# Performance work log

Measured on AMD Instinct MI355X. Metric: run time of the kernel, lower is better.

Reference implementation:

```python
import jax, jax.numpy as jnp
import numpy as np

N, IN, D, H, L, G, FF, E = 50000, 100, 128, 8, 3, 64, 512, 800000


def setup_inputs() -> dict:
    key = jax.random.key(0)
    ks = jax.random.split(key, 12)
    s = 0.02
    x = jax.random.normal(ks[0], (N, IN), dtype=jnp.float32)
    edge_index = jax.random.randint(ks[1], (2, E), 0, N)
    batch = jnp.sort(jax.random.randint(ks[2], (N,), 0, G))
    emb_W = jax.random.normal(ks[3], (IN, D), dtype=jnp.float32) * s
    Wqk = jax.random.normal(ks[4], (L, D, 2 * D), dtype=jnp.float32) * s
    Wv = jax.random.normal(ks[5], (L, D, D), dtype=jnp.float32) * s
    Wo = jax.random.normal(ks[6], (L, D, D), dtype=jnp.float32) * s
    bo = jnp.zeros((L, D), dtype=jnp.float32)
    W1 = jax.random.normal(ks[7], (L, D, FF), dtype=jnp.float32) * s
    b1 = jnp.zeros((L, FF), dtype=jnp.float32)
    W2 = jax.random.normal(ks[8], (L, FF, D), dtype=jnp.float32) * s
    b2 = jnp.zeros((L, D), dtype=jnp.float32)
    return {"x": x, "emb_W": emb_W, "Wqk": Wqk, "Wv": Wv, "Wo": Wo, "bo": bo,
            "W1": W1, "b1": b1, "W2": W2, "b2": b2,
            "edge_index": edge_index, "batch": batch}


def reference(x, emb_W, Wqk, Wv, Wo, bo, W1, b1, W2, b2, edge_index, batch):
    n = x.shape[0]
    d = emb_W.shape[1]
    n_layers = Wqk.shape[0]
    n_heads = H
    hd = d // n_heads
    scale = hd ** (-0.5)
    src, dst = edge_index[0], edge_index[1]  # PyG: j=source, i=target

    h = x @ emb_W  # [n, d]  (dropout is identity in eval)
    for l in range(n_layers):
        qk = h @ Wqk[l]  # [n, 2d]; chunk0 -> _j (source), chunk1 -> _i (target)
        q = qk[:, :d].reshape(n, n_heads, hd)
        k = qk[:, d:].reshape(n, n_heads, hd)
        v = (h @ Wv[l]).reshape(n, n_heads, hd)
        # per-edge attention scores [E, H]
        scores = jnp.sum(k[dst] * q[src], axis=-1) * scale
        # segment softmax over edges sharing a destination node
        m = jax.ops.segment_max(scores, dst, num_segments=n)
        ex = jnp.exp(scores - m[dst])
        denom = jax.ops.segment_sum(ex, dst, num_segments=n)
        attn = ex / (denom[dst] + 1e-16)  # utils.softmax adds 1e-16
        msg = v[src] * attn[:, :, None]  # [E, H, hd]
        out = jax.ops.segment_sum(msg, dst, num_segments=n).reshape(n, d)
        out = out @ Wo[l] + bo[l]
        h = h + out  # norm1 = Identity (batch_norm=True)
        ff = jax.nn.relu(h @ W1[l] + b1[l]) @ W2[l] + b2[l]
        h = h + ff  # norm2 = Identity
    # global mean pool per graph
    n_graphs = G
    sums = jax.ops.segment_sum(h, batch, num_segments=n_graphs)
    cnt = jax.ops.segment_sum(jnp.ones((n, 1), h.dtype), batch, num_segments=n_graphs)
    return sums / jnp.maximum(cnt, 1.0)
```

## Files before the change

kernel.cpp:

```cpp
#include <hip/hip_runtime.h>
#include <math.h>

#define NN 50000
#define NPAD 50048
#define IN_DIM 100
#define DD 128
#define HH 8
#define LL 3
#define GG 64
#define FFD 512
#define EE 800000

typedef __attribute__((ext_vector_type(8))) short bf8_t;
typedef __attribute__((ext_vector_type(4))) float f4_t;

static __device__ __forceinline__ unsigned short f2bf(float f) {
    unsigned u = __builtin_bit_cast(unsigned, f);
    unsigned r = (u + 0x7FFFu + ((u >> 16) & 1u)) >> 16;
    return (unsigned short)r;
}
static __device__ __forceinline__ float bf2f(unsigned short b) {
    unsigned u = ((unsigned)b) << 16;
    return __builtin_bit_cast(float, u);
}

#define GLD16(gsrc, ldst) __builtin_amdgcn_global_load_lds( \
    (const __attribute__((address_space(1))) unsigned int*)(gsrc), \
    (__attribute__((address_space(3))) unsigned int*)(ldst), 16, 0, 0)

__global__ __launch_bounds__(256) void mfma_gemm(
    const unsigned short* __restrict__ Ac,
    const unsigned short* __restrict__ Bc,
    const float* __restrict__ bias,
    const float* __restrict__ resid,
    float* __restrict__ Cf,
    unsigned short* __restrict__ Chl,
    unsigned short* __restrict__ Cb,
    int n, int nk, int M, int do_relu, int a_plain)
{
    __shared__ unsigned short ldsA[128 * 64];
    __shared__ unsigned short ldsB[128 * 64];
    const int tid = threadIdx.x;
    const int lane = tid & 63;
    const int wid = tid >> 6;
    const int wr = (wid >> 1) * 64;
    const int wc = (wid & 1) * 64;
    const long brow = (long)blockIdx.x * 128;
    const long bcol = (long)blockIdx.y * 128;

    f4_t acc[4][4] = {};

    const int srow = tid >> 3;
    const int kbg = (((tid & 7) << 4) ^ ((srow & 7) << 4)) >> 1;
    const int fr = lane & 15;
    const int kq = (lane >> 4) << 4;
    const int kq4 = lane >> 4;

    for (int kc = 0; kc < nk; ++kc) {
        if (a_plain) {
#pragma unroll
            for (int i = 0; i < 2; ++i) {
                int lin = i * 256 + tid;
                int row = lin >> 2, sd = lin & 3;
                GLD16(Ac + (brow + row) * (size_t)(nk * 32) + kc * 32 + ((sd ^ (row & 3)) << 3),
                      &ldsA[(size_t)lin * 8]);
            }
        } else {
#pragma unroll
            for (int i = 0; i < 4; ++i) {
                int row = i * 32 + srow;
                GLD16(Ac + ((brow + row) * (size_t)nk + kc) * 64 + kbg,
                      &ldsA[((size_t)i * 256 + tid) * 8]);
            }
        }
#pragma unroll
        for (int i = 0; i < 4; ++i) {
            int row = i * 32 + srow;
            GLD16(Bc + ((bcol + row) * (size_t)nk + kc) * 64 + kbg,
                  &ldsB[((size_t)i * 256 + tid) * 8]);
        }
        __syncthreads();

        bf8_t bh[4], bl[4];
#pragma unroll
        for (int nn = 0; nn < 4; ++nn) {
            int row = wc + nn * 16 + fr;
            int sw = (row & 7) << 4;
            bh[nn] = *(const bf8_t*)&ldsB[row * 64 + ((kq ^ sw) >> 1)];
            bl[nn] = *(const bf8_t*)&ldsB[row * 64 + (((kq + 64) ^ sw) >> 1)];
        }
        if (a_plain) {
            bf8_t ah[4];
#pragma unroll
            for (int m = 0; m < 4; ++m) {
                int row = wr + m * 16 + fr;
                ah[m] = *(const bf8_t*)&ldsA[row * 32 + ((kq4 ^ (row & 3)) << 3)];
            }
#pragma unroll
            for (int m = 0; m < 4; ++m)
#pragma unroll
                for (int nn = 0; nn < 4; ++nn) {
                    acc[m][nn] = __builtin_amdgcn_mfma_f32_16x16x32_bf16(ah[m], bh[nn], acc[m][nn], 0, 0, 0);
                    acc[m][nn] = __builtin_amdgcn_mfma_f32_16x16x32_bf16(ah[m], bl[nn], acc[m][nn], 0, 0, 0);
                }
        } else {
            bf8_t ah[4], al[4];
#pragma unroll
            for (int m = 0; m < 4; ++m) {
                int row = wr + m * 16 + fr;
                int sw = (row & 7) << 4;
                ah[m] = *(const bf8_t*)&ldsA[row * 64 + ((kq ^ sw) >> 1)];
                al[m] = *(const bf8_t*)&ldsA[row * 64 + (((kq + 64) ^ sw) >> 1)];
            }
#pragma unroll
            for (int m = 0; m < 4; ++m)
#pragma unroll
                for (int nn = 0; nn < 4; ++nn) {
                    acc[m][nn] = __builtin_amdgcn_mfma_f32_16x16x32_bf16(ah[m], bh[nn], acc[m][nn], 0, 0, 0);
                    acc[m][nn] = __builtin_amdgcn_mfma_f32_16x16x32_bf16(al[m], bh[nn], acc[m][nn], 0, 0, 0);
                    acc[m][nn] = __builtin_amdgcn_mfma_f32_16x16x32_bf16(ah[m], bl[nn], acc[m][nn], 0, 0, 0);
                }
        }
        __syncthreads();
    }

    const int efr = lane & 15, efq = lane >> 4;
#pragma unroll
    for (int m = 0; m < 4; ++m) {
#pragma unroll
        for (int i = 0; i < 4; ++i) {
            long row = brow + wr + m * 16 + efq * 4 + i;
            if (row >= n) continue;
#pragma unroll
            for (int nn = 0; nn < 4; ++nn) {
                int col = (int)bcol + wc + nn * 16 + efr;
                float v = acc[m][nn][i];
                if (bias) v += bias[col];
                if (do_relu) v = fmaxf(v, 0.f);
                if (resid) v += resid[row * M + col];
                if (Cf) Cf[row * M + col] = v;
                if (Cb) Cb[row * M + col] = f2bf(v);
                if (Chl) {
                    unsigned short hb = f2bf(v);
                    float lo = v - bf2f(hb);
                    size_t cb = (row * (size_t)(M >> 5) + (col >> 5)) * 64 + (col & 31);
                    Chl[cb] = hb;
                    Chl[cb + 32] = f2bf(lo);
                }
            }
        }
    }
}

__global__ __launch_bounds__(256, 3) void ff_fused(
    const unsigned short* __restrict__ hcin,
    const unsigned short* __restrict__ W1T,
    const unsigned short* __restrict__ W2T,
    const float* __restrict__ b1,
    const float* __restrict__ b2,
    float* __restrict__ h,
    unsigned short* __restrict__ hcout,
    int n)
{
    __shared__ unsigned short ldsA[64 * 32];
    __shared__ unsigned short ldsB[128 * 64];
    __shared__ unsigned short midb[64 * 128];

    const int tid = threadIdx.x;
    const int lane = tid & 63;
    const int wid = tid >> 6;
    const int wr = (wid >> 1) * 32;
    const int wc = (wid & 1) * 64;
    const long brow = (long)blockIdx.x * 64;

    const int srow = tid >> 3;
    const int kbg = (((tid & 7) << 4) ^ ((srow & 7) << 4)) >> 1;
    const int fr = lane & 15;
    const int kq = (lane >> 4) << 4;
    const int kq4 = lane >> 4;
    const int efr = lane & 15, efq = lane >> 4;

    f4_t acc2[2][4] = {};

    for (int c = 0; c < 4; ++c) {
        f4_t acc1[2][4] = {};
        for (int kc = 0; kc < 4; ++kc) {
            {
                int row = tid >> 2, sd = tid & 3;
                GLD16(hcin + ((brow + row) * (size_t)4 + kc) * 64 + ((sd ^ (row & 3)) << 3),
                      &ldsA[(size_t)tid * 8]);
            }
#pragma unroll
            for (int i = 0; i < 4; ++i) {
                int row = i * 32 + srow;
                GLD16(W1T + (((size_t)c * 128 + row) * 4 + kc) * 64 + kbg,
                      &ldsB[((size_t)i * 256 + tid) * 8]);
            }
            __syncthreads();
            bf8_t ah[2], bh[4], bl[4];
#pragma unroll
            for (int m = 0; m < 2; ++m) {
                int row = wr + m * 16 + fr;
                ah[m] = *(const bf8_t*)&ldsA[row * 32 + ((kq4 ^ (row & 3)) << 3)];
            }
#pragma unroll
            for (int nn = 0; nn < 4; ++nn) {
                int rowb = wc + nn * 16 + fr;
                int sw = (rowb & 7) << 4;
                bh[nn] = *(const bf8_t*)&ldsB[rowb * 64 + ((kq ^ sw) >> 1)];
                bl[nn] = *(const bf8_t*)&ldsB[rowb * 64 + (((kq + 64) ^ sw) >> 1)];
            }
#pragma unroll
            for (int m = 0; m < 2; ++m)
#pragma unroll
                for (int nn = 0; nn < 4; ++nn) {
                    acc1[m][nn] = __builtin_amdgcn_mfma_f32_16x16x32_bf16(ah[m], bh[nn], acc1[m][nn], 0, 0, 0);
                    acc1[m][nn] = __builtin_amdgcn_mfma_f32_16x16x32_bf16(ah[m], bl[nn], acc1[m][nn], 0, 0, 0);
                }
            __syncthreads();
        }
#pragma unroll
        for (int m = 0; m < 2; ++m)
#pragma unroll
            for (int i = 0; i < 4; ++i) {
                int lrow = wr + m * 16 + efq * 4 + i;
#pragma unroll
                for (int nn = 0; nn < 4; ++nn) {
                    int col = wc + nn * 16 + efr;
                    float v = fmaxf(acc1[m][nn][i] + b1[c * 128 + col], 0.f);
                    int e = (lrow << 7) + ((((col << 1) ^ ((lrow & 7) << 4))) >> 1);
                    midb[e] = f2bf(v);
                }
            }
        __syncthreads();
        for (int kq2 = 0; kq2 < 4; ++kq2) {
            int kcp = c * 4 + kq2;
#pragma unroll
            for (int i = 0; i < 4; ++i) {
                int row = i * 32 + srow;
                GLD16(W2T + ((size_t)row * 16 + kcp) * 64 + kbg,
                      &ldsB[((size_t)i * 256 + tid) * 8]);
            }
            __syncthreads();
            bf8_t am[2], bh2[4], bl2[4];
#pragma unroll
            for (int m = 0; m < 2; ++m) {
                int lrow = wr + m * 16 + fr;
                int kbyte = (kq2 * 64 + kq) ^ ((lrow & 7) << 4);
                am[m] = *(const bf8_t*)&midb[(lrow << 7) + (kbyte >> 1)];
            }
#pragma unroll
            for (int nn = 0; nn < 4; ++nn) {
                int rowb = wc + nn * 16 + fr;
                int sw = (rowb & 7) << 4;
                bh2[nn] = *(const bf8_t*)&ldsB[rowb * 64 + ((kq ^ sw) >> 1)];
                bl2[nn] = *(const bf8_t*)&ldsB[rowb * 64 + (((kq + 64) ^ sw) >> 1)];
            }
#pragma unroll
            for (int m = 0; m < 2; ++m)
#pragma unroll
                for (int nn = 0; nn < 4; ++nn) {
                    acc2[m][nn] = __builtin_amdgcn_mfma_f32_16x16x32_bf16(am[m], bh2[nn], acc2[m][nn], 0, 0, 0);
                    acc2[m][nn] = __builtin_amdgcn_mfma_f32_16x16x32_bf16(am[m], bl2[nn], acc2[m][nn], 0, 0, 0);
                }
            __syncthreads();
        }
    }

#pragma unroll
    for (int m = 0; m < 2; ++m)
#pragma unroll
        for (int i = 0; i < 4; ++i) {
            long row = brow + wr + m * 16 + efq * 4 + i;
            if (row >= n) continue;
#pragma unroll
            for (int nn = 0; nn < 4; ++nn) {
                int col = wc + nn * 16 + efr;
                float v = acc2[m][nn][i] + b2[col] + h[row * 128 + col];
                h[row * 128 + col] = v;
                if (hcout) {
                    unsigned short hb = f2bf(v);
                    size_t cb = (row * (size_t)4 + (col >> 5)) * 64 + (col & 31);
                    hcout[cb] = hb;
                    hcout[cb + 32] = f2bf(v - bf2f(hb));
                }
            }
        }
}

__global__ void cvt_x_kernel(const float* __restrict__ x, unsigned short* __restrict__ xc)
{
    int idx = blockIdx.x * 256 + threadIdx.x;
    if (idx >= NN * 128) return;
    int node = idx >> 7, col = idx & 127;
    float v = (col < IN_DIM) ? x[(size_t)node * IN_DIM + col] : 0.f;
    unsigned short hb = f2bf(v);
    float lo = v - bf2f(hb);
    size_t b = (size_t)node * 256 + (col >> 5) * 64 + (col & 31);
    xc[b] = hb;
    xc[b + 32] = f2bf(lo);
}

struct WDesc { const float* W; unsigned short* Wt; int K, nkpad, M, base; };
struct WDescs { WDesc d[16]; int n; int total; };

__global__ void wcvt_all_kernel(WDescs ds)
{
    int idx = blockIdx.x * 256 + threadIdx.x;
    if (idx >= ds.total) return;
    int di = 0;
    while (di + 1 < ds.n && idx >= ds.d[di + 1].base) ++di;
    WDesc w = ds.d[di];
    int loc = idx - w.base;
    int m = loc % w.M;
    int kc = loc / w.M;
    size_t ob = ((size_t)m * w.nkpad + kc) * 64;
    for (int i = 0; i < 32; ++i) {
        int k = kc * 32 + i;
        float v = (k < w.K) ? w.W[(size_t)k * w.M + m] : 0.f;
        unsigned short hb = f2bf(v);
        w.Wt[ob + i] = hb;
        w.Wt[ob + 32 + i] = f2bf(v - bf2f(hb));
    }
}

__global__ void count_kernel(const int* __restrict__ dst, int* __restrict__ counts)
{
    int e = blockIdx.x * 256 + threadIdx.x;
    if (e < EE) atomicAdd(&counts[dst[e]], 1);
}

__global__ __launch_bounds__(1024) void scan1_kernel(
    const int* __restrict__ counts, int* __restrict__ offsets, int* __restrict__ bsums)
{
    __shared__ int buf[1024];
    int tid = threadIdx.x;
    int i = blockIdx.x * 1024 + tid;
    int v = (i < NN) ? counts[i] : 0;
    buf[tid] = v;
    __syncthreads();
    for (int off = 1; off < 1024; off <<= 1) {
        int t = (tid >= off) ? buf[tid - off] : 0;
        __syncthreads();
        buf[tid] += t;
        __syncthreads();
    }
    if (i < NN) offsets[i + 1] = buf[tid];
    if (tid == 1023) bsums[blockIdx.x] = buf[1023];
}

__global__ void scan2_kernel(int* __restrict__ bsums, int nb)
{
    __shared__ int buf[64];
    int tid = threadIdx.x;
    int v = (tid < nb) ? bsums[tid] : 0;
    buf[tid] = v;
    __syncthreads();
    for (int off = 1; off < 64; off <<= 1) {
        int t = (tid >= off) ? buf[tid - off] : 0;
        __syncthreads();
        buf[tid] += t;
        __syncthreads();
    }
    if (tid < nb) bsums[tid] = buf[tid] - v;
}

__global__ __launch_bounds__(1024) void scan3_kernel(
    int* __restrict__ offsets, const int* __restrict__ bsums)
{
    int i = blockIdx.x * 1024 + threadIdx.x;
    if (i < NN) offsets[i + 1] += bsums[blockIdx.x];
    if (i == 0) offsets[0] = 0;
}

__global__ void fill_kernel(const int* __restrict__ src, const int* __restrict__ dst,
                            const int* __restrict__ offsets, int* __restrict__ cursor,
                            int* __restrict__ csr_src)
{
    int e = blockIdx.x * 256 + threadIdx.x;
    if (e < EE) {
        int d = dst[e];
        int pos = atomicAdd(&cursor[d], 1);
        csr_src[offsets[d] + pos] = src[e];
    }
}

__global__ __launch_bounds__(256) void attn_kernel(
    const unsigned short* __restrict__ QKV,
    const int* __restrict__ offsets, const int* __restrict__ csr_src,
    unsigned short* __restrict__ ac)
{
    int wave = threadIdx.x >> 6;
    int lane = threadIdx.x & 63;
    int node = blockIdx.x * 4 + wave;
    if (node >= NN) return;
    int qoff = ((lane >> 3) << 4) + ((lane & 7) << 1);
    ushort2 k2 = *(const ushort2*)&QKV[(size_t)node * 384 + 128 + qoff];
    float kx = bf2f(k2.x), ky = bf2f(k2.y);
    float m = -INFINITY, s = 0.f, a0 = 0.f, a1 = 0.f;
    int e = offsets[node], end = offsets[node + 1];
    for (; e + 3 < end; e += 4) {
        int j0 = csr_src[e], j1 = csr_src[e + 1], j2 = csr_src[e + 2], j3 = csr_src[e + 3];
        ushort2 q0 = *(const ushort2*)&QKV[(size_t)j0 * 384 + qoff];
        ushort2 q1 = *(const ushort2*)&QKV[(size_t)j1 * 384 + qoff];
        ushort2 q2 = *(const ushort2*)&QKV[(size_t)j2 * 384 + qoff];
        ushort2 q3 = *(const ushort2*)&QKV[(size_t)j3 * 384 + qoff];
        ushort2 v0 = *(const ushort2*)&QKV[(size_t)j0 * 384 + 256 + qoff];
        ushort2 v1 = *(const ushort2*)&QKV[(size_t)j1 * 384 + 256 + qoff];
        ushort2 v2 = *(const ushort2*)&QKV[(size_t)j2 * 384 + 256 + qoff];
        ushort2 v3 = *(const ushort2*)&QKV[(size_t)j3 * 384 + 256 + qoff];
        float p0 = kx * bf2f(q0.x) + ky * bf2f(q0.y);
        float p1 = kx * bf2f(q1.x) + ky * bf2f(q1.y);
        float p2 = kx * bf2f(q2.x) + ky * bf2f(q2.y);
        float p3 = kx * bf2f(q3.x) + ky * bf2f(q3.y);
        p0 += __shfl_xor(p0, 1, 64); p0 += __shfl_xor(p0, 2, 64); p0 += __shfl_xor(p0, 4, 64);
        p1 += __shfl_xor(p1, 1, 64); p1 += __shfl_xor(p1, 2, 64); p1 += __shfl_xor(p1, 4, 64);
        p2 += __shfl_xor(p2, 1, 64); p2 += __shfl_xor(p2, 2, 64); p2 += __shfl_xor(p2, 4, 64);
        p3 += __shfl_xor(p3, 1, 64); p3 += __shfl_xor(p3, 2, 64); p3 += __shfl_xor(p3, 4, 64);
        float sc0 = p0 * 0.25f, sc1 = p1 * 0.25f, sc2 = p2 * 0.25f, sc3 = p3 * 0.25f;
        float mx = fmaxf(fmaxf(fmaxf(sc0, sc1), fmaxf(sc2, sc3)), m);
        float corr = __expf(m - mx);
        float w0 = __expf(sc0 - mx), w1 = __expf(sc1 - mx);
        float w2 = __expf(sc2 - mx), w3 = __expf(sc3 - mx);
        s  = s  * corr + (w0 + w1) + (w2 + w3);
        a0 = a0 * corr + w0 * bf2f(v0.x) + w1 * bf2f(v1.x) + w2 * bf2f(v2.x) + w3 * bf2f(v3.x);
        a1 = a1 * corr + w0 * bf2f(v0.y) + w1 * bf2f(v1.y) + w2 * bf2f(v2.y) + w3 * bf2f(v3.y);
        m = mx;
    }
    if (e + 1 < end) {
        int j0 = csr_src[e], j1 = csr_src[e + 1];
        ushort2 q0 = *(const ushort2*)&QKV[(size_t)j0 * 384 + qoff];
        ushort2 v0 = *(const ushort2*)&QKV[(size_t)j0 * 384 + 256 + qoff];
        ushort2 q1 = *(const ushort2*)&QKV[(size_t)j1 * 384 + qoff];
        ushort2 v1 = *(const ushort2*)&QKV[(size_t)j1 * 384 + 256 + qoff];
        float p0 = kx * bf2f(q0.x) + ky * bf2f(q0.y);
        float p1 = kx * bf2f(q1.x) + ky * bf2f(q1.y);
        p0 += __shfl_xor(p0, 1, 64); p0 += __shfl_xor(p0, 2, 64); p0 += __shfl_xor(p0, 4, 64);
        p1 += __shfl_xor(p1, 1, 64); p1 += __shfl_xor(p1, 2, 64); p1 += __shfl_xor(p1, 4, 64);
        float sc0 = p0 * 0.25f, sc1 = p1 * 0.25f;
        float mn = fmaxf(m, fmaxf(sc0, sc1));
        float corr = __expf(m - mn);
        float w0 = __expf(sc0 - mn), w1 = __expf(sc1 - mn);
        s  = s  * corr + w0 + w1;
        a0 = a0 * corr + w0 * bf2f(v0.x) + w1 * bf2f(v1.x);
        a1 = a1 * corr + w0 * bf2f(v0.y) + w1 * bf2f(v1.y);
        m = mn;
        e += 2;
    }
    if (e < end) {
        int j = csr_src[e];
        ushort2 qj = *(const ushort2*)&QKV[(size_t)j * 384 + qoff];
        ushort2 vj = *(const ushort2*)&QKV[(size_t)j * 384 + 256 + qoff];
        float p = kx * bf2f(qj.x) + ky * bf2f(qj.y);
        p += __shfl_xor(p, 1, 64); p += __shfl_xor(p, 2, 64); p += __shfl_xor(p, 4, 64);
        float score = p * 0.25f;
        float mn = fmaxf(m, score);
        float corr = __expf(m - mn);
        float w = __expf(score - mn);
        s  = s  * corr + w;
        a0 = a0 * corr + w * bf2f(vj.x);
        a1 = a1 * corr + w * bf2f(vj.y);
        m = mn;
    }
    float inv = 1.f / (s + 1e-16f);
    ushort2 o;
    o.x = f2bf(a0 * inv);
    o.y = f2bf(a1 * inv);
    *(ushort2*)&ac[(size_t)node * 128 + qoff] = o;
}

__global__ __launch_bounds__(256) void pool_kernel(
    const float* __restrict__ h, const int* __restrict__ batch,
    float* __restrict__ sums, int* __restrict__ cnts)
{
    int tid = threadIdx.x;
    int c4 = tid & 31;
    int rs = tid >> 5;
    int start = blockIdx.x * 256;
    int r0 = start + rs;
    if (r0 >= NN) return;
    int lim = min(start + 256, NN);
    float4 acc = make_float4(0.f, 0.f, 0.f, 0.f);
    int cnt = 0;
    int cur = batch[r0];
    for (int r = r0; r < lim; r += 8) {
        int g = batch[r];
        if (g != cur) {
            atomicAdd(&sums[cur * DD + c4 * 4 + 0], acc.x);
            atomicAdd(&sums[cur * DD + c4 * 4 + 1], acc.y);
            atomicAdd(&sums[cur * DD + c4 * 4 + 2], acc.z);
            atomicAdd(&sums[cur * DD + c4 * 4 + 3], acc.w);
            if (c4 == 0) atomicAdd(&cnts[cur], cnt);
            acc = make_float4(0.f, 0.f, 0.f, 0.f);
            cnt = 0; cur = g;
        }
        float4 v = *(const float4*)&h[(size_t)r * DD + c4 * 4];
        acc.x += v.x; acc.y += v.y; acc.z += v.z; acc.w += v.w;
        ++cnt;
    }
    atomicAdd(&sums[cur * DD + c4 * 4 + 0], acc.x);
    atomicAdd(&sums[cur * DD + c4 * 4 + 1], acc.y);
    atomicAdd(&sums[cur * DD + c4 * 4 + 2], acc.z);
    atomicAdd(&sums[cur * DD + c4 * 4 + 3], acc.w);
    if (c4 == 0) atomicAdd(&cnts[cur], cnt);
}

__global__ void finalize_kernel(const float* __restrict__ sums, const int* __restrict__ cnts,
                                float* __restrict__ out)
{
    int g = blockIdx.x, c = threadIdx.x;
    out[g * DD + c] = sums[g * DD + c] / fmaxf((float)cnts[g], 1.f);
}

extern "C" void kernel_launch(void* const* d_in, const int* in_sizes, int n_in,
                              void* d_out, int out_size, void* d_ws, size_t ws_size,
                              hipStream_t stream)
{
    const float* x     = (const float*)d_in[0];
    const float* emb_W = (const float*)d_in[1];
    const float* Wqk   = (const float*)d_in[2];
    const float* Wv    = (const float*)d_in[3];
    const float* Wo    = (const float*)d_in[4];
    const float* bo    = (const float*)d_in[5];
    const float* W1    = (const float*)d_in[6];
    const float* b1    = (const float*)d_in[7];
    const float* W2    = (const float*)d_in[8];
    const float* b2    = (const float*)d_in[9];
    const int* eidx    = (const int*)d_in[10];
    const int* batch   = (const int*)d_in[11];
    float* out = (float*)d_out;

    char* base = (char*)d_ws;
    size_t off = 0;
    auto alloc = [&](size_t bytes) { char* p = base + off; off = (off + bytes + 255) & ~(size_t)255; return p; };

    float*          h    = (float*)alloc((size_t)NPAD * DD * 4);
    unsigned short* hc   = (unsigned short*)alloc((size_t)NPAD * 2 * DD * 2);
    char*           regB = alloc((size_t)NPAD * 384 * 2 + (size_t)NPAD * 128 * 2 + 256);
    unsigned short* xc   = (unsigned short*)regB;
    unsigned short* QKVb = (unsigned short*)regB;
    unsigned short* acp  = (unsigned short*)(regB + (size_t)NPAD * 384 * 2);

    unsigned short* WqkvT = (unsigned short*)alloc((size_t)LL * 384 * 256 * 2);
    unsigned short* WoT   = (unsigned short*)alloc((size_t)LL * 128 * 256 * 2);
    unsigned short* W1T   = (unsigned short*)alloc((size_t)LL * 512 * 256 * 2);
    unsigned short* W2T   = (unsigned short*)alloc((size_t)LL * 128 * 1024 * 2);
    unsigned short* embT  = (unsigned short*)alloc((size_t)128 * 256 * 2);

    int* counts  = (int*)alloc((NN + 1) * 4);
    int* offsets = (int*)alloc((NN + 1) * 4);
    int* cursor  = (int*)alloc(NN * 4);
    int* bsums   = (int*)alloc(64 * 4);
    int* csr_src = (int*)alloc((size_t)EE * 4);
    float* sums  = (float*)alloc(GG * DD * 4 + GG * 4);
    int* cnts    = (int*)(sums + GG * DD);

    const int* src = eidx;
    const int* dst = eidx + EE;

    hipMemsetAsync(counts, 0, (NN + 1) * sizeof(int), stream);
    hipMemsetAsync(cursor, 0, NN * sizeof(int), stream);
    hipMemsetAsync(sums, 0, GG * DD * sizeof(float) + GG * sizeof(int), stream);

    const int NB1 = (NN + 1023) / 1024;
    count_kernel<<<dim3((EE + 255) / 256), dim3(256), 0, stream>>>(dst, counts);
    scan1_kernel<<<dim3(NB1), dim3(1024), 0, stream>>>(counts, offsets, bsums);
    scan2_kernel<<<dim3(1), dim3(64), 0, stream>>>(bsums, NB1);
    scan3_kernel<<<dim3(NB1), dim3(1024), 0, stream>>>(offsets, bsums);
    fill_kernel<<<dim3((EE + 255) / 256), dim3(256), 0, stream>>>(src, dst, offsets, cursor, csr_src);

    WDescs ds;
    int b = 0, di = 0;
    auto addw = [&](const float* W, unsigned short* Wt, int K, int nkpad, int M) {
        ds.d[di].W = W; ds.d[di].Wt = Wt; ds.d[di].K = K;
        ds.d[di].nkpad = nkpad; ds.d[di].M = M; ds.d[di].base = b;
        b += M * nkpad; ++di;
    };
    addw(emb_W, embT, IN_DIM, 4, DD);
    for (int l = 0; l < LL; ++l) {
        addw(Wqk + (size_t)l * DD * 256, WqkvT + (size_t)l * 384 * 256, DD, 4, 256);
        addw(Wv  + (size_t)l * DD * DD,  WqkvT + (size_t)l * 384 * 256 + 256 * 256, DD, 4, 128);
        addw(Wo  + (size_t)l * DD * DD,  WoT + (size_t)l * 128 * 256, DD, 4, 128);
        addw(W1  + (size_t)l * DD * FFD, W1T + (size_t)l * 512 * 256, DD, 4, 512);
        addw(W2  + (size_t)l * FFD * DD, W2T + (size_t)l * 128 * 1024, FFD, 16, 128);
    }
    ds.n = di; ds.total = b;
    wcvt_all_kernel<<<dim3((b + 255) / 256), dim3(256), 0, stream>>>(ds);

    cvt_x_kernel<<<dim3((NN * 128 + 255) / 256), dim3(256), 0, stream>>>(x, xc);

    dim3 blk(256);
    const int gx = (NN + 127) / 128;
    const int gx2 = (NN + 63) / 64;

    mfma_gemm<<<dim3(gx, 1), blk, 0, stream>>>(
        xc, embT, nullptr, nullptr, h, hc, nullptr, NN, 4, DD, 0, 0);

    for (int l = 0; l < LL; ++l) {
        mfma_gemm<<<dim3(gx, 3), blk, 0, stream>>>(
            hc, WqkvT + (size_t)l * 384 * 256, nullptr, nullptr,
            nullptr, nullptr, QKVb, NN, 4, 384, 0, 0);
        attn_kernel<<<dim3(NN / 4), blk, 0, stream>>>(QKVb, offsets, csr_src, acp);
        mfma_gemm<<<dim3(gx, 1), blk, 0, stream>>>(
            acp, WoT + (size_t)l * 128 * 256, bo + (size_t)l * DD, h,
            h, hc, nullptr, NN, 4, DD, 0, 1);
        ff_fused<<<dim3(gx2), blk, 0, stream>>>(
            hc, W1T + (size_t)l * 512 * 256, W2T + (size_t)l * 128 * 1024,
            b1 + (size_t)l * FFD, b2 + (size_t)l * DD, h,
            (l == LL - 1) ? nullptr : hc, NN);
    }

    pool_kernel<<<dim3((NN + 255) / 256), blk, 0, stream>>>(h, batch, sums, cnts);
    finalize_kernel<<<dim3(GG), dim3(128), 0, stream>>>(sums, cnts, out);
}
```

Before: 902.8 us.

## Double-buffer weight tiles and keep activations in registers in fused FFN

Restructures the fused FFN kernel into a single fully unrolled 32-step loop. The weight tiles are double-buffered in LDS, so the next W1/W2 tile is prefetched while MFMAs run on the current one, and each step needs one barrier instead of two. The input activation fragments are now loaded once into registers straight from global memory rather than staged through LDS on every k-chunk. The costs are higher register pressure from the preloaded A fragments and full unrolling, plus 16KB more LDS, which may hurt occupancy at 3 blocks per CU.

```diff
diff --git a/kernel.cpp b/kernel.cpp
--- a/kernel.cpp
+++ b/kernel.cpp
@@ -152,6 +152,18 @@
     }
 }
 
+#define FF_STAGE(T, BUF) do {                                                   \
+    const int c_ = (T) >> 3, ph_ = ((T) >> 2) & 1, j_ = (T) & 3;                \
+    _Pragma("unroll")                                                           \
+    for (int i_ = 0; i_ < 4; ++i_) {                                            \
+        int row_ = i_ * 32 + srow;                                              \
+        const unsigned short* srcp_ = (ph_ == 0)                                \
+            ? W1T + (((size_t)c_ * 128 + row_) * 4 + j_) * 64 + kbg             \
+            : W2T + ((size_t)row_ * 16 + (c_ * 4 + j_)) * 64 + kbg;             \
+        GLD16(srcp_, &ldsB[BUF][((size_t)i_ * 256 + tid) * 8]);                 \
+    }                                                                           \
+} while (0)
+
 __global__ __launch_bounds__(256, 3) void ff_fused(
     const unsigned short* __restrict__ hcin,
     const unsigned short* __restrict__ W1T,
@@ -162,8 +174,7 @@
     unsigned short* __restrict__ hcout,
     int n)
 {
-    __shared__ unsigned short ldsA[64 * 32];
-    __shared__ unsigned short ldsB[128 * 64];
+    __shared__ unsigned short ldsB[2][128 * 64];
     __shared__ unsigned short midb[64 * 128];
 
     const int tid = threadIdx.x;
@@ -180,81 +191,89 @@
     const int kq4 = lane >> 4;
     const int efr = lane & 15, efq = lane >> 4;
 
-    f4_t acc2[2][4] = {};
-
-    for (int c = 0; c < 4; ++c) {
-        f4_t acc1[2][4] = {};
-        for (int kc = 0; kc < 4; ++kc) {
-            {
-                int row = tid >> 2, sd = tid & 3;
-                GLD16(hcin + ((brow + row) * (size_t)4 + kc) * 64 + ((sd ^ (row & 3)) << 3),
-                      &ldsA[(size_t)tid * 8]);
-            }
-#pragma unroll
-            for (int i = 0; i < 4; ++i) {
-                int row = i * 32 + srow;
-                GLD16(W1T + (((size_t)c * 128 + row) * 4 + kc) * 64 + kbg,
-                      &ldsB[((size_t)i * 256 + tid) * 8]);
-            }
-            __syncthreads();
-            bf8_t ah[2], bh[4], bl[4];
-#pragma unroll
-            for (int m = 0; m < 2; ++m) {
-                int row = wr + m * 16 + fr;
-                ah[m] = *(const bf8_t*)&ldsA[row * 32 + ((kq4 ^ (row & 3)) << 3)];
-            }
+    bf8_t ahr[2][4];
+#pragma unroll
+    for (int m = 0; m < 2; ++m) {
+        long arow = brow + wr + m * 16 + fr;
+#pragma unroll
+        for (int kc = 0; kc < 4; ++kc)
+            ahr[m][kc] = *(const bf8_t*)&hcin[(arow * 4 + kc) * (size_t)64 + kq4 * 8];
+    }
+
+    FF_STAGE(0, 0);
+
+    f4_t acc1[2][4];
+    f4_t acc2[2][4];
+#pragma unroll
+    for (int m = 0; m < 2; ++m)
+#pragma unroll
+        for (int nn = 0; nn < 4; ++nn) {
+            acc2[m][nn][0] = 0.f; acc2[m][nn][1] = 0.f;
+            acc2[m][nn][2] = 0.f; acc2[m][nn][3] = 0.f;
+        }
+
+    __syncthreads();
+
+#pragma unroll
+    for (int t = 0; t < 32; ++t) {
+        const int c = t >> 3, ph = (t >> 2) & 1, j = t & 3;
+        const int cur = t & 1;
+        if (t < 31) FF_STAGE(t + 1, cur ^ 1);
+
+        if (ph == 0) {
+            if (j == 0) {
+#pragma unroll
+                for (int m = 0; m < 2; ++m)
+#pragma unroll
+                    for (int nn = 0; nn < 4; ++nn) {
+                        acc1[m][nn][0] = 0.f; acc1[m][nn][1] = 0.f;
+                        acc1[m][nn][2] = 0.f; acc1[m][nn][3] = 0.f;
+                    }
+            }
+            bf8_t bh[4], bl[4];
 #pragma unroll
             for (int nn = 0; nn < 4; ++nn) {
                 int rowb = wc + nn * 16 + fr;
                 int sw = (rowb & 7) << 4;
-                bh[nn] = *(const bf8_t*)&ldsB[rowb * 64 + ((kq ^ sw) >> 1)];
-                bl[nn] = *(const bf8_t*)&ldsB[rowb * 64 + (((kq + 64) ^ sw) >> 1)];
+                bh[nn] = *(const bf8_t*)&ldsB[cur][rowb * 64 + ((kq ^ sw) >> 1)];
+                bl[nn] = *(const bf8_t*)&ldsB[cur][rowb * 64 + (((kq + 64) ^ sw) >> 1)];
             }
 #pragma unroll
             for (int m = 0; m < 2; ++m)
 #pragma unroll
                 for (int nn = 0; nn < 4; ++nn) {
-                    acc1[m][nn] = __builtin_amdgcn_mfma_f32_16x16x32_bf16(ah[m], bh[nn], acc1[m][nn], 0, 0, 0);
-                    acc1[m][nn] = __builtin_amdgcn_mfma_f32_16x16x32_bf16(ah[m], bl[nn], acc1[m][nn], 0, 0, 0);
+                    acc1[m][nn] = __builtin_amdgcn_mfma_f32_16x16x32_bf16(ahr[m][j], bh[nn], acc1[m][nn], 0, 0, 0);
+                    acc1[m][nn] = __builtin_amdgcn_mfma_f32_16x16x32_bf16(ahr[m][j], bl[nn], acc1[m][nn], 0, 0, 0);
                 }
-            __syncthreads();
-        }
-#pragma unroll
-        for (int m = 0; m < 2; ++m)
-#pragma unroll
-            for (int i = 0; i < 4; ++i) {
-                int lrow = wr + m * 16 + efq * 4 + i;
-#pragma unroll
-                for (int nn = 0; nn < 4; ++nn) {
-                    int col = wc + nn * 16 + efr;
-                    float v = fmaxf(acc1[m][nn][i] + b1[c * 128 + col], 0.f);
-                    int e = (lrow << 7) + ((((col << 1) ^ ((lrow & 7) << 4))) >> 1);
-                    midb[e] = f2bf(v);
-                }
-            }
-        __syncthreads();
-        for (int kq2 = 0; kq2 < 4; ++kq2) {
-            int kcp = c * 4 + kq2;
-#pragma unroll
-            for (int i = 0; i < 4; ++i) {
-                int row = i * 32 + srow;
-                GLD16(W2T + ((size_t)row * 16 + kcp) * 64 + kbg,
-                      &ldsB[((size_t)i * 256 + tid) * 8]);
-            }
-            __syncthreads();
+            if (j == 3) {
+#pragma unroll
+                for (int m = 0; m < 2; ++m)
+#pragma unroll
+                    for (int i = 0; i < 4; ++i) {
+                        int lrow = wr + m * 16 + efq * 4 + i;
+#pragma unroll
+                        for (int nn = 0; nn < 4; ++nn) {
+                            int col = wc + nn * 16 + efr;
+                            float v = fmaxf(acc1[m][nn][i] + b1[c * 128 + col], 0.f);
+                            int e2 = (lrow << 7) + ((((col << 1) ^ ((lrow & 7) << 4))) >> 1);
+                            midb[e2] = f2bf(v);
+                        }
+                    }
+            }
+        } else {
             bf8_t am[2], bh2[4], bl2[4];
 #pragma unroll
             for (int m = 0; m < 2; ++m) {
                 int lrow = wr + m * 16 + fr;
-                int kbyte = (kq2 * 64 + kq) ^ ((lrow & 7) << 4);
+                int kbyte = (j * 64 + kq) ^ ((lrow & 7) << 4);
                 am[m] = *(const bf8_t*)&midb[(lrow << 7) + (kbyte >> 1)];
             }
 #pragma unroll
             for (int nn = 0; nn < 4; ++nn) {
                 int rowb = wc + nn * 16 + fr;
                 int sw = (rowb & 7) << 4;
-                bh2[nn] = *(const bf8_t*)&ldsB[rowb * 64 + ((kq ^ sw) >> 1)];
-                bl2[nn] = *(const bf8_t*)&ldsB[rowb * 64 + (((kq + 64) ^ sw) >> 1)];
+                bh2[nn] = *(const bf8_t*)&ldsB[cur][rowb * 64 + ((kq ^ sw) >> 1)];
+                bl2[nn] = *(const bf8_t*)&ldsB[cur][rowb * 64 + (((kq + 64) ^ sw) >> 1)];
             }
 #pragma unroll
             for (int m = 0; m < 2; ++m)
@@ -263,8 +282,8 @@
                     acc2[m][nn] = __builtin_amdgcn_mfma_f32_16x16x32_bf16(am[m], bh2[nn], acc2[m][nn], 0, 0, 0);
                     acc2[m][nn] = __builtin_amdgcn_mfma_f32_16x16x32_bf16(am[m], bl2[nn], acc2[m][nn], 0, 0, 0);
                 }
-            __syncthreads();
-        }
+        }
+        __syncthreads();
     }
 
 #pragma unroll
```

Measured after the change: 932.5 us. +3.3%, slower.
